# Kernel tuning notes

Measured on AMD Instinct MI355X. Metric: run time of the kernel, lower is better.

The kernel has to match this reference:

```python
import jax, jax.numpy as jnp
import numpy as np

CONF_THRES = 0.4
IOU_THRES = 0.45
MAX_WH = 4096.0   # class offset for class-aware NMS (agnostic=False)
MAX_DET = 300
B, N, NC = 8, 25200, 80


def setup_inputs() -> dict:
    key = jax.random.key(0)
    k1, k2, k3, k4, k5 = jax.random.split(key, 5)
    # realistic raw detector output: xywh in pixels, obj/cls scores in [0,1]
    xy = jax.random.uniform(k1, (B, N, 2), minval=0.0, maxval=608.0)
    wh = jax.random.uniform(k2, (B, N, 2), minval=4.0, maxval=96.0)
    obj = jax.random.uniform(k3, (B, N, 1))
    cls = jax.random.uniform(k4, (B, N, NC))
    prediction = jnp.concatenate([xy, wh, obj, cls], axis=-1)  # [B,N,85]
    logits = jax.random.normal(k5, (B, N, NC))
    return {"prediction": prediction, "logits": logits}


def _xywh2xyxy(b):
    cx, cy, w, h = b[..., 0], b[..., 1], b[..., 2], b[..., 3]
    return jnp.stack([cx - w / 2, cy - h / 2, cx + w / 2, cy + h / 2], axis=-1)


def _iou_one_vs_all(box, boxes):
    # box [4], boxes [N,4] -> IoU [N]
    lt = jnp.maximum(box[:2], boxes[:, :2])
    rb = jnp.minimum(box[2:], boxes[:, 2:])
    wh = jnp.clip(rb - lt, 0.0)
    inter = wh[:, 0] * wh[:, 1]
    a1 = (box[2] - box[0]) * (box[3] - box[1])
    a2 = (boxes[:, 2] - boxes[:, 0]) * (boxes[:, 3] - boxes[:, 1])
    return inter / (a1 + a2 - inter + 1e-9)


def _nms_image(pred, log_):
    # pred [N, 5+NC], log_ [N, NC]
    obj = pred[:, 4]
    scores_all = pred[:, 5:] * obj[:, None]          # x[:,5:] *= x[:,4:5]
    conf = scores_all.max(-1)                        # best-class conf
    cls = jnp.argmax(scores_all, -1)
    # obj-conf prefilter (xc mask) AND final conf filter, expressed as masking
    valid = (obj > CONF_THRES) & (conf > CONF_THRES)
    box = _xywh2xyxy(pred[:, :4])                    # [N,4]
    obox = box + (cls.astype(box.dtype) * MAX_WH)[:, None]  # class offset
    score0 = jnp.where(valid, conf, -1.0)

    def step(score_cur, _):
        idx = jnp.argmax(score_cur)
        keep = score_cur[idx] > 0.0
        iou = _iou_one_vs_all(obox[idx], obox)
        # suppress everything with IoU > thr (includes the picked box itself)
        new_score = jnp.where(keep & (iou > IOU_THRES), -1.0, score_cur)
        return new_score, (idx, keep)

    _, (idxs, keeps) = jax.lax.scan(step, score0, None, length=MAX_DET)
    m = keeps.astype(box.dtype)[:, None]
    dets = jnp.concatenate(
        [box[idxs], conf[idxs, None], cls[idxs, None].astype(box.dtype)], axis=-1
    ) * m                                            # [MAX_DET, 6], zero-padded
    return dets, log_[idxs] * m, keeps


def reference(prediction, logits):
    # returns (dets [B,300,6] = xyxy,conf,cls ; logits_sel [B,300,80] ; keep mask [B,300])
    return jax.vmap(_nms_image)(prediction, logits)
```

## Files before the change

kernel.cpp:

```cpp
#include <hip/hip_runtime.h>

#pragma clang fp contract(off)

#define NB 8
#define NN 25200
#define NCLS 80
#define NSTR 85
#define MAXDET 300
#define CONF_T 0.4f
#define IOU_T 0.45f
#define MAX_WH_C 4096.0f

#define NBIN 1024
#define BINSHIFT 14
#define BINBASE 0x3EC00000u
#define SELN 512
#define SORTN 2048

typedef unsigned long long ull;

__device__ __forceinline__ float cand_score(const float* __restrict__ p) {
    float obj = p[4];
    float best = p[5] * obj;
    for (int j = 1; j < NCLS; ++j) {
        float s = p[5 + j] * obj;
        if (s > best) best = s;
    }
    return ((obj > CONF_T) && (best > CONF_T)) ? best : -1.0f;
}
__device__ __forceinline__ int cand_cls(const float* __restrict__ p) {
    float obj = p[4];
    float best = p[5] * obj; int bc = 0;
    for (int j = 1; j < NCLS; ++j) {
        float s = p[5 + j] * obj;
        if (s > best) { best = s; bc = j; }
    }
    return bc;
}
__device__ __forceinline__ bool iou_gt(float ax1, float ay1, float ax2, float ay2, float aarea,
                                       float bx1, float by1, float bx2, float by2, float barea) {
    float lx = fmaxf(ax1, bx1);
    float ly = fmaxf(ay1, by1);
    float rx = fminf(ax2, bx2);
    float ry = fminf(ay2, by2);
    float iw = fmaxf(rx - lx, 0.0f);
    float ih = fmaxf(ry - ly, 0.0f);
    float inter = iw * ih;
    float iou = inter / ((aarea + barea - inter) + 1e-9f);
    return iou > IOU_T;
}

#define PREP_ROWS 64
__global__ __launch_bounds__(256) void prep_kernel(const float* __restrict__ pred,
                                                   float* __restrict__ score_ws) {
    __shared__ float st[PREP_ROWS * NSTR];
    const int R0 = blockIdx.x * PREP_ROWS;
    const float4* src = reinterpret_cast<const float4*>(pred + (size_t)R0 * NSTR);
    float4* dst4 = reinterpret_cast<float4*>(st);
    const int tid = threadIdx.x;
    for (int i = tid; i < PREP_ROWS * NSTR / 4; i += 256) dst4[i] = src[i];
    __syncthreads();

    int row = tid >> 2, part = tid & 3;
    const float* pr = st + row * NSTR;
    float obj = pr[4];
    float best = -1.0f;
    const float* pc = pr + 5 + part * 20;
#pragma unroll
    for (int k = 0; k < 20; ++k) {
        float s = pc[k] * obj;
        if (s > best) best = s;
    }
#pragma unroll
    for (int d = 1; d <= 2; d <<= 1) {
        float ob = __shfl_xor(best, d);
        if (ob > best) best = ob;
    }
    if (part == 0) {
        int grow = R0 + row;
        bool valid = (obj > CONF_T) && (best > CONF_T);
        score_ws[grow] = valid ? best : -1.0f;
    }
}

__global__ __launch_bounds__(1024) void selimg_kernel(const float* __restrict__ pred,
                                                      const float* __restrict__ score_ws,
                                                      int* __restrict__ cnt_ws, int* __restrict__ total_ws,
                                                      ull* __restrict__ sel_key,
                                                      float* __restrict__ sel_x1, float* __restrict__ sel_y1,
                                                      float* __restrict__ sel_x2, float* __restrict__ sel_y2,
                                                      float* __restrict__ sel_area, float* __restrict__ sel_cls,
                                                      int* __restrict__ sel_idx) {
    __shared__ int s_hist[NBIN];
    __shared__ ull s_key[SELN];
    __shared__ int s_gidx[SELN];
    __shared__ int s_cnt, s_T, s_total;

    const int b = blockIdx.x;
    const int tid = threadIdx.x;
    const int lane = tid & 63;
    const int wid = tid >> 6;
    const float* predb = pred + (size_t)b * NN * NSTR;
    const float* sb = score_ws + (size_t)b * NN;

    s_hist[tid] = 0;
    if (tid == 0) s_cnt = 0;
    __syncthreads();
    for (int g = tid; g < NN; g += 1024) {
        float s = sb[g];
        if (s > 0.0f) {
            int bin = (int)((__float_as_uint(s) - BINBASE) >> BINSHIFT);
            atomicAdd(&s_hist[bin], 1);
        }
    }
    __syncthreads();

    if (wid == 0) {
        int acc = 0; int S[16];
#pragma unroll
        for (int k = 15; k >= 0; --k) { acc += s_hist[lane * 16 + k]; S[k] = acc; }
        int tot = acc;
        int incl = tot;
#pragma unroll
        for (int d = 1; d < 64; d <<= 1) {
            int v = __shfl_down(incl, d);
            if (lane + d < 64) incl += v;
        }
        int E = incl - tot;
        int Tl = NBIN;
#pragma unroll
        for (int k = 0; k < 16; ++k)
            if (Tl == NBIN && S[k] + E <= SELN) Tl = lane * 16 + k;
        int total0 = incl;
#pragma unroll
        for (int d = 1; d < 64; d <<= 1) {
            int o = __shfl_xor(Tl, d);
            if (o < Tl) Tl = o;
        }
        if (lane == 0) { s_T = Tl; s_total = total0; }
    }
    __syncthreads();
    int T = s_T;

    for (int g = tid; g < NN; g += 1024) {
        float s = sb[g];
        if (s > 0.0f) {
            int bin = (int)((__float_as_uint(s) - BINBASE) >> BINSHIFT);
            if (bin >= T) {
                int pos = atomicAdd(&s_cnt, 1);
                if (pos < SELN) {
                    s_key[pos] = ((ull)__float_as_uint(s) << 32)
                                 | (unsigned int)(0xFFFFFFFFu - (unsigned int)g);
                    s_gidx[pos] = g;
                }
            }
        }
    }
    __syncthreads();
    int cnt = s_cnt; if (cnt > SELN) cnt = SELN;

    if (tid < cnt) {
        int g = s_gidx[tid];
        const float* p = predb + (size_t)g * NSTR;
        float cx = p[0], cy = p[1], w = p[2], h = p[3];
        int c = cand_cls(p);
        float off = (float)c * MAX_WH_C;
        float x1 = (cx - w * 0.5f) + off;
        float y1 = (cy - h * 0.5f) + off;
        float x2 = (cx + w * 0.5f) + off;
        float y2 = (cy + h * 0.5f) + off;
        int o = b * SELN + tid;
        sel_key[o] = s_key[tid];
        sel_x1[o] = x1; sel_y1[o] = y1; sel_x2[o] = x2; sel_y2[o] = y2;
        sel_area[o] = (x2 - x1) * (y2 - y1);
        sel_cls[o] = (float)c;
        sel_idx[o] = g;
    }
    if (tid == 0) { cnt_ws[b] = cnt; total_ws[b] = s_total; }
}

__global__ __launch_bounds__(256) void mask_kernel(const int* __restrict__ cnt_ws,
                                                   const ull* __restrict__ sel_key,
                                                   const float* __restrict__ sel_x1, const float* __restrict__ sel_y1,
                                                   const float* __restrict__ sel_x2, const float* __restrict__ sel_y2,
                                                   const float* __restrict__ sel_area,
                                                   ull* __restrict__ mask_ws) {
    __shared__ ull skey[SELN];
    __shared__ float ox1[SELN], oy1[SELN], ox2[SELN], oy2[SELN], oar[SELN];
    const int b = blockIdx.x >> 4;
    const int chunk = blockIdx.x & 15;
    const int tid = threadIdx.x;
    int cnt = cnt_ws[b]; if (cnt > SELN) cnt = SELN;
    for (int s = tid; s < SELN; s += 256) {
        if (s < cnt) {
            skey[s] = sel_key[b * SELN + s];
            ox1[s] = sel_x1[b * SELN + s]; oy1[s] = sel_y1[b * SELN + s];
            ox2[s] = sel_x2[b * SELN + s]; oy2[s] = sel_y2[b * SELN + s];
            oar[s] = sel_area[b * SELN + s];
        } else skey[s] = 0ull;
    }
    __syncthreads();
    int i = chunk * 32 + (tid & 31);
    int w = tid >> 5;
    if (i < cnt) {
        ull ki = skey[i];
        float ax1 = ox1[i], ay1 = oy1[i], ax2 = ox2[i], ay2 = oy2[i], aar = oar[i];
        ull m = 0ull;
        int jb = w << 6;
        int jend = cnt - jb; if (jend > 64) jend = 64;
        for (int t = 0; t < jend; ++t) {
            int j = jb + t;
            bool s = (skey[j] > ki) && iou_gt(ax1, ay1, ax2, ay2, aar,
                                             ox1[j], oy1[j], ox2[j], oy2[j], oar[j]);
            m |= (ull)s << t;
        }
        mask_ws[b * (8 * SELN) + w * SELN + i] = m;
    }
}

__global__ __launch_bounds__(1024) void resolve_kernel(
        const float* __restrict__ pred, const float* __restrict__ logits,
        const float* __restrict__ score_ws,
        const int* __restrict__ cnt_ws, const int* __restrict__ total_ws,
        const ull* __restrict__ mask_ws, const ull* __restrict__ sel_key,
        const float* __restrict__ sel_x1, const float* __restrict__ sel_y1,
        const float* __restrict__ sel_x2, const float* __restrict__ sel_y2,
        const float* __restrict__ sel_area, const float* __restrict__ sel_cls,
        const int* __restrict__ sel_idx,
        float* __restrict__ out) {
    __shared__ ull s_m[8][SELN];
    __shared__ ull s_key[SELN];
    __shared__ ull s_kw[8];
    __shared__ ull s_minkey;
    __shared__ float s_x1[SELN], s_y1[SELN], s_x2[SELN], s_y2[SELN], s_ar[SELN], s_cl[SELN];
    __shared__ int s_ix[SELN];
    __shared__ float kx1[MAXDET], ky1[MAXDET], kx2[MAXDET], ky2[MAXDET], kar[MAXDET];
    __shared__ float ksc[MAXDET], kcl[MAXDET];
    __shared__ int kix[MAXDET];
    __shared__ int s_kc;

    const int b = blockIdx.x;
    const int tid = threadIdx.x;
    const int lane = tid & 63;
    const int wid = tid >> 6;
    const float* predb = pred + (size_t)b * NN * NSTR;
    const float* logb  = logits + (size_t)b * NN * NCLS;
    const float* sb    = score_ws + (size_t)b * NN;

    int cnt = cnt_ws[b]; if (cnt > SELN) cnt = SELN;

    for (int i = tid; i < 8 * SELN; i += 1024)
        (&s_m[0][0])[i] = mask_ws[b * (8 * SELN) + i];
    for (int s = tid; s < SELN; s += 1024) {
        if (s < cnt) {
            s_key[s] = sel_key[b * SELN + s];
            s_x1[s] = sel_x1[b * SELN + s]; s_y1[s] = sel_y1[b * SELN + s];
            s_x2[s] = sel_x2[b * SELN + s]; s_y2[s] = sel_y2[b * SELN + s];
            s_ar[s] = sel_area[b * SELN + s]; s_cl[s] = sel_cls[b * SELN + s];
            s_ix[s] = sel_idx[b * SELN + s];
        } else s_key[s] = 0ull;
    }
    __syncthreads();

    if (wid == 0) {
        ull mk = ~0ull;
#pragma unroll
        for (int r = 0; r < 8; ++r) {
            int i = (r << 6) + lane;
            if (i < cnt) { ull k = s_key[i]; if (k < mk) mk = k; }
        }
#pragma unroll
        for (int d = 32; d >= 1; d >>= 1) {
            ull o = __shfl_xor(mk, d);
            if (o < mk) mk = o;
        }
        if (lane == 0) s_minkey = mk;

        ull vm[8], kw[8];
#pragma unroll
        for (int r = 0; r < 8; ++r) {
            int lo = r << 6;
            vm[r] = (cnt >= lo + 64) ? ~0ull : (cnt > lo ? ((1ull << (cnt - lo)) - 1ull) : 0ull);
            kw[r] = vm[r];
        }
        for (int round = 0; round < SELN; ++round) {
            ull nw[8];
#pragma unroll
            for (int r = 0; r < 8; ++r) {
                int i = (r << 6) + lane;
                ull supp = 0ull;
#pragma unroll
                for (int w = 0; w < 8; ++w) supp |= kw[w] & s_m[w][i];
                nw[r] = __ballot((int)(supp == 0ull)) & vm[r];
            }
            bool changed = false;
#pragma unroll
            for (int r = 0; r < 8; ++r) { changed |= (nw[r] != kw[r]); kw[r] = nw[r]; }
            if (!changed) break;
        }
        int totkept = 0;
#pragma unroll
        for (int r = 0; r < 8; ++r) totkept += __popcll(kw[r]);
        if (lane == 0) { s_kc = totkept < MAXDET ? totkept : MAXDET; }
        if (lane < 8) s_kw[lane] = kw[lane];
    }
    __syncthreads();
    int kc = s_kc;

    if (tid < SELN) {
        bool kept = (s_kw[tid >> 6] >> (tid & 63)) & 1ull;
        if (!kept) s_key[tid] = 0ull;
    }
    __syncthreads();

    {
        int i = tid >> 1, half = tid & 1;
        ull k = s_key[i];
        int r = 0;
        if (k != 0ull) {
            int jb = half << 8;
            for (int jj = 0; jj < 256; ++jj) {
                ull kj = s_key[jb + jj];
                r += (int)(kj > k);
            }
        }
        r += __shfl_xor(r, 1);
        if (half == 0 && k != 0ull && r < MAXDET) {
            kx1[r] = s_x1[i]; ky1[r] = s_y1[i]; kx2[r] = s_x2[i]; ky2[r] = s_y2[i];
            kar[r] = s_ar[i]; ksc[r] = __uint_as_float((unsigned int)(k >> 32));
            kcl[r] = s_cl[i]; kix[r] = s_ix[i];
        }
    }
    __syncthreads();

    if (wid == 0 && kc < MAXDET && total_ws[b] > cnt) {
        ull prevkey = (cnt > 0) ? s_minkey : ~0ull;
        while (kc < MAXDET) {
            ull best = 0ull;
            for (int i0 = lane; i0 < NN; i0 += 64) {
                float s = sb[i0];
                if (s > 0.0f) {
                    ull key = ((ull)__float_as_uint(s) << 32)
                              | (unsigned int)(0xFFFFFFFFu - (unsigned int)i0);
                    if (key < prevkey && key > best) best = key;
                }
            }
#pragma unroll
            for (int d = 32; d >= 1; d >>= 1) {
                ull o = __shfl_xor(best, d);
                if (o > best) best = o;
            }
            if (best == 0ull) break;
            prevkey = best;
            int gi = (int)(0xFFFFFFFFu - (unsigned int)(best & 0xFFFFFFFFull));
            float sc = __uint_as_float((unsigned int)(best >> 32));
            const float* pp = predb + (size_t)gi * NSTR;
            float cx = pp[0], cy = pp[1], w = pp[2], h = pp[3];
            int c = cand_cls(pp);
            float off = (float)c * MAX_WH_C;
            float x1 = (cx - w * 0.5f) + off;
            float y1 = (cy - h * 0.5f) + off;
            float x2 = (cx + w * 0.5f) + off;
            float y2 = (cy + h * 0.5f) + off;
            float ar = (x2 - x1) * (y2 - y1);
            bool f = false;
            for (int t = lane; t < kc; t += 64)
                if (iou_gt(kx1[t], ky1[t], kx2[t], ky2[t], kar[t], x1, y1, x2, y2, ar)) f = true;
            if (!__any((int)f)) {
                if (lane == 0) {
                    kx1[kc] = x1; ky1[kc] = y1; kx2[kc] = x2; ky2[kc] = y2;
                    kar[kc] = ar; ksc[kc] = sc; kcl[kc] = (float)c; kix[kc] = gi;
                }
                kc++;
            }
        }
        if (lane == 0) s_kc = kc;
    }
    __syncthreads();
    kc = s_kc;

    if (tid < MAXDET) {
        int t = tid;
        float o0 = 0, o1 = 0, o2 = 0, o3 = 0, o4 = 0, o5 = 0;
        if (t < kc) {
            int idx = kix[t];
            const float* pp = predb + (size_t)idx * NSTR;
            float cx = pp[0], cy = pp[1], w = pp[2], h = pp[3];
            o0 = cx - w * 0.5f; o1 = cy - h * 0.5f;
            o2 = cx + w * 0.5f; o3 = cy + h * 0.5f;
            o4 = ksc[t];        o5 = kcl[t];
        }
        float* dd = out + (size_t)b * (MAXDET * 6) + (size_t)t * 6;
        dd[0] = o0; dd[1] = o1; dd[2] = o2; dd[3] = o3; dd[4] = o4; dd[5] = o5;
        out[(size_t)NB * MAXDET * 6 + (size_t)NB * MAXDET * NCLS + (size_t)b * MAXDET + t] =
            (t < kc) ? 1.0f : 0.0f;
    }
    float* lbase = out + (size_t)NB * MAXDET * 6 + (size_t)b * (MAXDET * NCLS);
    for (int t = wid; t < MAXDET; t += 16) {
        float* dst = lbase + (size_t)t * NCLS;
        if (t < kc) {
            const float* src = logb + (size_t)kix[t] * NCLS;
            for (int c = lane; c < NCLS; c += 64) dst[c] = src[c];
        } else {
            for (int c = lane; c < NCLS; c += 64) dst[c] = 0.0f;
        }
    }
}

__global__ __launch_bounds__(1024) void fallback_kernel(const float* __restrict__ pred,
                                                        const float* __restrict__ logits,
                                                        float* __restrict__ out) {
    __shared__ ull s_keys[SORTN];
    __shared__ float sel_x1[SORTN], sel_y1[SORTN], sel_x2[SORTN], sel_y2[SORTN];
    __shared__ float sel_area[SORTN], sel_cls[SORTN];
    __shared__ int   sel_idx[SORTN];
    __shared__ float kx1[MAXDET], ky1[MAXDET], kx2[MAXDET], ky2[MAXDET], karea[MAXDET];
    __shared__ float kscore[MAXDET], kcls[MAXDET];
    __shared__ int   kidx[MAXDET];
    __shared__ int   s_hist[NBIN];
    __shared__ int   s_suppk[64];
    __shared__ unsigned int s_supmask[64][2];
    __shared__ int   s_kc, s_T, s_cnt;

    const int b = blockIdx.x;
    const int tid = threadIdx.x;
    const int lane = tid & 63;
    const int wid = tid >> 6;
    const float* predb = pred + (size_t)b * NN * NSTR;
    const float* logb  = logits + (size_t)b * NN * NCLS;

    int kc_total = 0;
    int prevT = NBIN;

    while (kc_total < MAXDET && prevT > 0) {
        s_hist[tid] = 0;
        if (tid == 0) { s_cnt = 0; s_T = NBIN; }
        __syncthreads();
        for (int i = tid; i < NN; i += 1024) {
            float s = cand_score(predb + (size_t)i * NSTR);
            if (s > 0.0f) {
                int bin = (int)((__float_as_uint(s) - BINBASE) >> BINSHIFT);
                if (bin < prevT) atomicAdd(&s_hist[bin], 1);
            }
        }
        __syncthreads();
        for (int d = 1; d < NBIN; d <<= 1) {
            int v = s_hist[tid] + ((tid + d < NBIN) ? s_hist[tid + d] : 0);
            __syncthreads();
            s_hist[tid] = v;
            __syncthreads();
        }
        if (s_hist[tid] <= SORTN) atomicMin(&s_T, tid);
        __syncthreads();
        int T = s_T;
        int rem_total = s_hist[0];
        if (T >= prevT) {
            if (rem_total == 0) { prevT = 0; break; }
            T = prevT - 1;
        }
        __syncthreads();
        for (int i = tid; i < NN; i += 1024) {
            float s = cand_score(predb + (size_t)i * NSTR);
            if (s > 0.0f) {
                int bin = (int)((__float_as_uint(s) - BINBASE) >> BINSHIFT);
                if (bin >= T && bin < prevT) {
                    int pos = atomicAdd(&s_cnt, 1);
                    if (pos < SORTN)
                        s_keys[pos] = ((ull)__float_as_uint(s) << 32)
                                      | (unsigned int)(0xFFFFFFFFu - (unsigned int)i);
                }
            }
        }
        __syncthreads();
        int cnt = s_cnt; if (cnt > SORTN) cnt = SORTN;
        int npow = 64; while (npow < cnt) npow <<= 1;
        for (int i = cnt + tid; i < npow; i += 1024) s_keys[i] = 0ull;
        __syncthreads();
        for (int k = 2; k <= npow; k <<= 1) {
            for (int j = k >> 1; j > 0; j >>= 1) {
                for (int idx = tid; idx < npow; idx += 1024) {
                    int p = idx ^ j;
                    if (p > idx) {
                        ull a = s_keys[idx], c = s_keys[p];
                        bool desc = ((idx & k) == 0);
                        if (desc ? (a < c) : (a > c)) { s_keys[idx] = c; s_keys[p] = a; }
                    }
                }
                __syncthreads();
            }
        }
        for (int t = tid; t < cnt; t += 1024) {
            ull key = s_keys[t];
            int i = (int)(0xFFFFFFFFu - (unsigned int)(key & 0xFFFFFFFFull));
            const float* p = predb + (size_t)i * NSTR;
            float cx = p[0], cy = p[1], w = p[2], h = p[3];
            int c = cand_cls(p);
            float off = (float)c * MAX_WH_C;
            float x1 = (cx - w * 0.5f) + off;
            float y1 = (cy - h * 0.5f) + off;
            float x2 = (cx + w * 0.5f) + off;
            float y2 = (cy + h * 0.5f) + off;
            sel_x1[t] = x1; sel_y1[t] = y1; sel_x2[t] = x2; sel_y2[t] = y2;
            sel_area[t] = (x2 - x1) * (y2 - y1);
            sel_cls[t] = (float)c;
            sel_idx[t] = i;
        }
        __syncthreads();
        int nb2 = (cnt + 63) >> 6;
        for (int batch = 0; batch < nb2; ++batch) {
            int kcb = kc_total;
            if (kcb >= MAXDET) break;
            if (tid < 64) { s_suppk[tid] = 0; s_supmask[tid][0] = 0u; s_supmask[tid][1] = 0u; }
            __syncthreads();

            int cloc = tid >> 4, ch = tid & 15;
            int gi = batch * 64 + cloc;
            bool validc = gi < cnt;
            float ax1 = 0, ay1 = 0, ax2 = 0, ay2 = 0, aar = 0;
            if (validc) {
                ax1 = sel_x1[gi]; ay1 = sel_y1[gi];
                ax2 = sel_x2[gi]; ay2 = sel_y2[gi]; aar = sel_area[gi];
            }
            bool flag = false;
            if (validc) {
                for (int t = ch; t < kcb; t += 16) {
                    if (iou_gt(kx1[t], ky1[t], kx2[t], ky2[t], karea[t],
                               ax1, ay1, ax2, ay2, aar)) flag = true;
                }
            }
            ull bal = __ballot((int)flag);
            if ((lane & 15) == 0) {
                unsigned int sub = (unsigned int)((bal >> (lane & 48)) & 0xFFFFull);
                s_suppk[cloc] = (sub != 0u);
            }
            unsigned int mbits = 0;
            if (validc) {
                for (int jj = 0; jj < 4; ++jj) {
                    int j = (ch << 2) + jj;
                    int gj = batch * 64 + j;
                    if (j > cloc && gj < cnt) {
                        if (iou_gt(ax1, ay1, ax2, ay2, aar,
                                   sel_x1[gj], sel_y1[gj], sel_x2[gj], sel_y2[gj], sel_area[gj]))
                            mbits |= 1u << (j & 31);
                    }
                }
            }
            if (mbits) atomicOr(&s_supmask[cloc][(ch >> 3) & 1], mbits);
            __syncthreads();

            if (wid == 0) {
                ull mask = ((ull)s_supmask[lane][1] << 32) | s_supmask[lane][0];
                bool validj = (batch * 64 + lane) < cnt;
                ull rem = __ballot((int)(validj && (s_suppk[lane] == 0)));
                ull keepbits = 0;
                int kcount = kcb;
                while (rem && kcount < MAXDET) {
                    int i = __builtin_ctzll(rem);
                    rem &= rem - 1;
                    keepbits |= 1ull << i;
                    ++kcount;
                    ull mi = __shfl(mask, i);
                    rem &= ~mi;
                }
                if ((keepbits >> lane) & 1ull) {
                    int pos = kcb + __popcll(keepbits & ((1ull << lane) - 1ull));
                    int g2 = batch * 64 + lane;
                    kx1[pos] = sel_x1[g2]; ky1[pos] = sel_y1[g2];
                    kx2[pos] = sel_x2[g2]; ky2[pos] = sel_y2[g2];
                    karea[pos] = sel_area[g2];
                    kcls[pos] = sel_cls[g2]; kidx[pos] = sel_idx[g2];
                    kscore[pos] = __uint_as_float((unsigned int)(s_keys[g2] >> 32));
                }
                if (lane == 0) s_kc = kcount;
            }
            __syncthreads();
            kc_total = s_kc;
            __syncthreads();
        }
        prevT = T;
    }

    __syncthreads();
    int kc = kc_total;
    if (tid < MAXDET) {
        int t = tid;
        float o0 = 0, o1 = 0, o2 = 0, o3 = 0, o4 = 0, o5 = 0;
        if (t < kc) {
            int idx = kidx[t];
            const float* pp = predb + (size_t)idx * NSTR;
            float cx = pp[0], cy = pp[1], w = pp[2], h = pp[3];
            o0 = cx - w * 0.5f; o1 = cy - h * 0.5f;
            o2 = cx + w * 0.5f; o3 = cy + h * 0.5f;
            o4 = kscore[t];     o5 = kcls[t];
        }
        float* dd = out + (size_t)b * (MAXDET * 6) + (size_t)t * 6;
        dd[0] = o0; dd[1] = o1; dd[2] = o2; dd[3] = o3; dd[4] = o4; dd[5] = o5;
        out[(size_t)NB * MAXDET * 6 + (size_t)NB * MAXDET * NCLS + (size_t)b * MAXDET + t] =
            (t < kc) ? 1.0f : 0.0f;
    }
    float* lbase = out + (size_t)NB * MAXDET * 6 + (size_t)b * (MAXDET * NCLS);
    for (int t = wid; t < MAXDET; t += 16) {
        float* dst = lbase + (size_t)t * NCLS;
        if (t < kc) {
            const float* src = logb + (size_t)kidx[t] * NCLS;
            for (int c = lane; c < NCLS; c += 64) dst[c] = src[c];
        } else {
            for (int c = lane; c < NCLS; c += 64) dst[c] = 0.0f;
        }
    }
}

extern "C" void kernel_launch(void* const* d_in, const int* in_sizes, int n_in,
                              void* d_out, int out_size, void* d_ws, size_t ws_size,
                              hipStream_t stream) {
    const float* pred   = (const float*)d_in[0];
    const float* logits = (const float*)d_in[1];
    float* out = (float*)d_out;

    const size_t off_mask = 0;
    const size_t off_key  = 262144;
    const size_t off_flt  = 294912;
    const size_t off_idx  = off_flt + 6 * 16384;
    const size_t off_cnt  = off_idx + 16384;
    const size_t off_tot  = off_cnt + 64;
    const size_t off_sws  = off_tot + 64;
    const size_t need     = off_sws + (size_t)NB * NN * 4;

    if (d_ws == nullptr || ws_size < need) {
        fallback_kernel<<<NB, 1024, 0, stream>>>(pred, logits, out);
        return;
    }

    char* ws = (char*)d_ws;
    ull* mask_ws = (ull*)(ws + off_mask);
    ull* sel_key = (ull*)(ws + off_key);
    float* sel_x1 = (float*)(ws + off_flt);
    float* sel_y1 = sel_x1 + NB * SELN;
    float* sel_x2 = sel_y1 + NB * SELN;
    float* sel_y2 = sel_x2 + NB * SELN;
    float* sel_area = sel_y2 + NB * SELN;
    float* sel_cls = sel_area + NB * SELN;
    int*   sel_idx = (int*)(ws + off_idx);
    int*   cnt_ws = (int*)(ws + off_cnt);
    int*   total_ws = (int*)(ws + off_tot);
    float* score_ws = (float*)(ws + off_sws);

    prep_kernel<<<(NB * NN) / PREP_ROWS, 256, 0, stream>>>(pred, score_ws);
    selimg_kernel<<<NB, 1024, 0, stream>>>(pred, score_ws, cnt_ws, total_ws, sel_key,
                                           sel_x1, sel_y1, sel_x2, sel_y2,
                                           sel_area, sel_cls, sel_idx);
    mask_kernel<<<NB * 16, 256, 0, stream>>>(cnt_ws, sel_key,
                                             sel_x1, sel_y1, sel_x2, sel_y2, sel_area, mask_ws);
    resolve_kernel<<<NB, 1024, 0, stream>>>(pred, logits, score_ws, cnt_ws, total_ws,
                                            mask_ws, sel_key,
                                            sel_x1, sel_y1, sel_x2, sel_y2,
                                            sel_area, sel_cls, sel_idx, out);
}
```

Before: 87.82 us.

## Fuse NMS pipeline into single cooperative persistent kernel with grid syncs

```diff
diff --git a/kernel.cpp b/kernel.cpp
--- a/kernel.cpp
+++ b/kernel.cpp
@@ -1,4 +1,5 @@
 #include <hip/hip_runtime.h>
+#include <hip/hip_cooperative_groups.h>
 
 #pragma clang fp contract(off)
 
@@ -16,8 +17,12 @@
 #define BINBASE 0x3EC00000u
 #define SELN 512
 #define SORTN 2048
+#define PREP_ROWS 64
+#define COOP_GRID 256
+#define COOP_BLK 256
 
 typedef unsigned long long ull;
+namespace cg = cooperative_groups;
 
 __device__ __forceinline__ float cand_score(const float* __restrict__ p) {
     float obj = p[4];
@@ -50,7 +55,351 @@
     return iou > IOU_T;
 }
 
-#define PREP_ROWS 64
+struct Params {
+    const float* pred; const float* logits;
+    float* score; int* hist; int* cnt; int* total;
+    ull* key; float* x1; float* y1; float* x2; float* y2; float* ar; float* cl; int* ix;
+    ull* mask; int* kix; float* ksc; float* kcl; int* kcnt;
+    float* out;
+};
+
+struct SMemA { float stage[PREP_ROWS * NSTR]; };
+struct SMemD { ull key[SELN]; float x1[SELN], y1[SELN], x2[SELN], y2[SELN], ar[SELN]; };
+struct SMemE {
+    ull m[8][SELN]; ull key[SELN];
+    float x1[SELN], y1[SELN], x2[SELN], y2[SELN], ar[SELN], cl[SELN];
+    int ix[SELN];
+    float kx1[MAXDET], ky1[MAXDET], kx2[MAXDET], ky2[MAXDET], kar[MAXDET], ksc[MAXDET], kcl[MAXDET];
+    int kix[MAXDET];
+};
+union SMem { SMemA a; SMemD d; SMemE e; };
+
+__global__ __launch_bounds__(COOP_BLK) void coop_kernel(Params P) {
+    __shared__ SMem sm;
+    __shared__ int sT, sTot, s_kc;
+    __shared__ ull s_kw[8];
+    __shared__ ull s_minkey;
+
+    cg::grid_group grid = cg::this_grid();
+    const int tid = threadIdx.x;
+    const int bx = blockIdx.x;
+
+    {
+        int gt = bx * COOP_BLK + tid;
+        for (int i = gt; i < NB * NBIN + NB; i += COOP_GRID * COOP_BLK) {
+            if (i < NB * NBIN) P.hist[i] = 0;
+            else P.cnt[i - NB * NBIN] = 0;
+        }
+    }
+    grid.sync();
+
+    for (int tile = bx; tile < (NB * NN) / PREP_ROWS; tile += COOP_GRID) {
+        const float4* src = reinterpret_cast<const float4*>(P.pred + (size_t)tile * PREP_ROWS * NSTR);
+        float4* dst4 = reinterpret_cast<float4*>(sm.a.stage);
+        for (int i = tid; i < PREP_ROWS * NSTR / 4; i += COOP_BLK) dst4[i] = src[i];
+        __syncthreads();
+        int row = tid >> 2, part = tid & 3;
+        const float* pr = sm.a.stage + row * NSTR;
+        float obj = pr[4];
+        float best = -1.0f;
+        const float* pc = pr + 5 + part * 20;
+#pragma unroll
+        for (int k = 0; k < 20; ++k) {
+            float s = pc[k] * obj;
+            if (s > best) best = s;
+        }
+#pragma unroll
+        for (int d = 1; d <= 2; d <<= 1) {
+            float ob = __shfl_xor(best, d);
+            if (ob > best) best = ob;
+        }
+        if (part == 0) {
+            int grow = tile * PREP_ROWS + row;
+            bool valid = (obj > CONF_T) && (best > CONF_T);
+            P.score[grow] = valid ? best : -1.0f;
+            if (valid) {
+                int ib = grow / NN;
+                int bin = (int)((__float_as_uint(best) - BINBASE) >> BINSHIFT);
+                atomicAdd(&P.hist[ib * NBIN + bin], 1);
+            }
+        }
+        __syncthreads();
+    }
+    grid.sync();
+
+    {
+        const int img = bx >> 5;
+        const int sub = bx & 31;
+        if (tid < 64) {
+            int lane = tid;
+            int acc = 0; int S[16];
+#pragma unroll
+            for (int k = 15; k >= 0; --k) { acc += P.hist[img * NBIN + lane * 16 + k]; S[k] = acc; }
+            int tot = acc;
+            int incl = tot;
+#pragma unroll
+            for (int d = 1; d < 64; d <<= 1) {
+                int v = __shfl_down(incl, d);
+                if (lane + d < 64) incl += v;
+            }
+            int E = incl - tot;
+            int Tl = NBIN;
+#pragma unroll
+            for (int k = 0; k < 16; ++k)
+                if (Tl == NBIN && S[k] + E <= SELN) Tl = lane * 16 + k;
+            int total0 = incl;
+#pragma unroll
+            for (int d = 1; d < 64; d <<= 1) {
+                int o = __shfl_xor(Tl, d);
+                if (o < Tl) Tl = o;
+            }
+            if (lane == 0) { sT = Tl; sTot = total0; }
+        }
+        __syncthreads();
+        int T = sT;
+        if (sub == 0 && tid == 0) P.total[img] = sTot;
+        const float* sb = P.score + (size_t)img * NN;
+        const float* predb = P.pred + (size_t)img * NN * NSTR;
+        int g0 = sub * 788;
+        int g1 = g0 + 788; if (g1 > NN) g1 = NN;
+        for (int g = g0 + tid; g < g1; g += COOP_BLK) {
+            float s = sb[g];
+            if (s > 0.0f) {
+                int bin = (int)((__float_as_uint(s) - BINBASE) >> BINSHIFT);
+                if (bin >= T) {
+                    int pos = atomicAdd(&P.cnt[img], 1);
+                    if (pos < SELN) {
+                        int o = img * SELN + pos;
+                        const float* p = predb + (size_t)g * NSTR;
+                        float cx = p[0], cy = p[1], w = p[2], h = p[3];
+                        int c = cand_cls(p);
+                        float off = (float)c * MAX_WH_C;
+                        float x1 = (cx - w * 0.5f) + off;
+                        float y1 = (cy - h * 0.5f) + off;
+                        float x2 = (cx + w * 0.5f) + off;
+                        float y2 = (cy + h * 0.5f) + off;
+                        P.key[o] = ((ull)__float_as_uint(s) << 32)
+                                   | (unsigned int)(0xFFFFFFFFu - (unsigned int)g);
+                        P.x1[o] = x1; P.y1[o] = y1; P.x2[o] = x2; P.y2[o] = y2;
+                        P.ar[o] = (x2 - x1) * (y2 - y1);
+                        P.cl[o] = (float)c; P.ix[o] = g;
+                    }
+                }
+            }
+        }
+    }
+    grid.sync();
+
+    if (bx < NB * 16) {
+        const int b = bx >> 4;
+        const int chunk = bx & 15;
+        int cntb = P.cnt[b]; if (cntb > SELN) cntb = SELN;
+        for (int s = tid; s < SELN; s += COOP_BLK) {
+            if (s < cntb) {
+                sm.d.key[s] = P.key[b * SELN + s];
+                sm.d.x1[s] = P.x1[b * SELN + s]; sm.d.y1[s] = P.y1[b * SELN + s];
+                sm.d.x2[s] = P.x2[b * SELN + s]; sm.d.y2[s] = P.y2[b * SELN + s];
+                sm.d.ar[s] = P.ar[b * SELN + s];
+            } else sm.d.key[s] = 0ull;
+        }
+        __syncthreads();
+        int i = chunk * 32 + (tid & 31);
+        int w = tid >> 5;
+        if (i < cntb) {
+            ull ki = sm.d.key[i];
+            float ax1 = sm.d.x1[i], ay1 = sm.d.y1[i], ax2 = sm.d.x2[i], ay2 = sm.d.y2[i], aar = sm.d.ar[i];
+            ull m = 0ull;
+            int jb = w << 6;
+            int jend = cntb - jb; if (jend > 64) jend = 64;
+            for (int t = 0; t < jend; ++t) {
+                int j = jb + t;
+                bool s = (sm.d.key[j] > ki) && iou_gt(ax1, ay1, ax2, ay2, aar,
+                                                     sm.d.x1[j], sm.d.y1[j], sm.d.x2[j], sm.d.y2[j], sm.d.ar[j]);
+                m |= (ull)s << t;
+            }
+            P.mask[b * (8 * SELN) + w * SELN + i] = m;
+        }
+    }
+    grid.sync();
+
+    if (bx < NB) {
+        const int b = bx;
+        const int lane = tid & 63;
+        const int wid = tid >> 6;
+        const float* predb = P.pred + (size_t)b * NN * NSTR;
+        const float* sb = P.score + (size_t)b * NN;
+        int cnt = P.cnt[b]; if (cnt > SELN) cnt = SELN;
+
+        for (int i = tid; i < 8 * SELN; i += COOP_BLK)
+            (&sm.e.m[0][0])[i] = P.mask[b * (8 * SELN) + i];
+        for (int s = tid; s < SELN; s += COOP_BLK) {
+            if (s < cnt) {
+                sm.e.key[s] = P.key[b * SELN + s];
+                sm.e.x1[s] = P.x1[b * SELN + s]; sm.e.y1[s] = P.y1[b * SELN + s];
+                sm.e.x2[s] = P.x2[b * SELN + s]; sm.e.y2[s] = P.y2[b * SELN + s];
+                sm.e.ar[s] = P.ar[b * SELN + s]; sm.e.cl[s] = P.cl[b * SELN + s];
+                sm.e.ix[s] = P.ix[b * SELN + s];
+            } else sm.e.key[s] = 0ull;
+        }
+        __syncthreads();
+
+        if (wid == 0) {
+            ull mk = ~0ull;
+#pragma unroll
+            for (int r = 0; r < 8; ++r) {
+                int i = (r << 6) + lane;
+                if (i < cnt) { ull k = sm.e.key[i]; if (k < mk) mk = k; }
+            }
+#pragma unroll
+            for (int d = 32; d >= 1; d >>= 1) {
+                ull o = __shfl_xor(mk, d);
+                if (o < mk) mk = o;
+            }
+            if (lane == 0) s_minkey = mk;
+
+            ull vm[8], kw[8];
+#pragma unroll
+            for (int r = 0; r < 8; ++r) {
+                int lo = r << 6;
+                vm[r] = (cnt >= lo + 64) ? ~0ull : (cnt > lo ? ((1ull << (cnt - lo)) - 1ull) : 0ull);
+                kw[r] = vm[r];
+            }
+            for (int round = 0; round < SELN; ++round) {
+                ull nw[8];
+#pragma unroll
+                for (int r = 0; r < 8; ++r) {
+                    int i = (r << 6) + lane;
+                    ull supp = 0ull;
+#pragma unroll
+                    for (int w = 0; w < 8; ++w) supp |= kw[w] & sm.e.m[w][i];
+                    nw[r] = __ballot((int)(supp == 0ull)) & vm[r];
+                }
+                bool changed = false;
+#pragma unroll
+                for (int r = 0; r < 8; ++r) { changed |= (nw[r] != kw[r]); kw[r] = nw[r]; }
+                if (!changed) break;
+            }
+            int totkept = 0;
+#pragma unroll
+            for (int r = 0; r < 8; ++r) totkept += __popcll(kw[r]);
+            if (lane == 0) s_kc = totkept < MAXDET ? totkept : MAXDET;
+            if (lane < 8) s_kw[lane] = kw[lane];
+        }
+        __syncthreads();
+        int kc = s_kc;
+
+        for (int s = tid; s < SELN; s += COOP_BLK) {
+            bool kept = (s_kw[s >> 6] >> (s & 63)) & 1ull;
+            if (!kept) sm.e.key[s] = 0ull;
+        }
+        __syncthreads();
+
+        for (int ii = tid; ii < SELN; ii += COOP_BLK) {
+            ull k = sm.e.key[ii];
+            if (k != 0ull) {
+                int r = 0;
+                for (int j = 0; j < SELN; ++j) r += (int)(sm.e.key[j] > k);
+                if (r < MAXDET) {
+                    sm.e.kx1[r] = sm.e.x1[ii]; sm.e.ky1[r] = sm.e.y1[ii];
+                    sm.e.kx2[r] = sm.e.x2[ii]; sm.e.ky2[r] = sm.e.y2[ii];
+                    sm.e.kar[r] = sm.e.ar[ii];
+                    sm.e.ksc[r] = __uint_as_float((unsigned int)(k >> 32));
+                    sm.e.kcl[r] = sm.e.cl[ii]; sm.e.kix[r] = sm.e.ix[ii];
+                }
+            }
+        }
+        __syncthreads();
+
+        if (wid == 0 && kc < MAXDET && P.total[b] > cnt) {
+            ull prevkey = (cnt > 0) ? s_minkey : ~0ull;
+            while (kc < MAXDET) {
+                ull best = 0ull;
+                for (int i0 = lane; i0 < NN; i0 += 64) {
+                    float s = sb[i0];
+                    if (s > 0.0f) {
+                        ull key = ((ull)__float_as_uint(s) << 32)
+                                  | (unsigned int)(0xFFFFFFFFu - (unsigned int)i0);
+                        if (key < prevkey && key > best) best = key;
+                    }
+                }
+#pragma unroll
+                for (int d = 32; d >= 1; d >>= 1) {
+                    ull o = __shfl_xor(best, d);
+                    if (o > best) best = o;
+                }
+                if (best == 0ull) break;
+                prevkey = best;
+                int gi = (int)(0xFFFFFFFFu - (unsigned int)(best & 0xFFFFFFFFull));
+                float sc = __uint_as_float((unsigned int)(best >> 32));
+                const float* pp = predb + (size_t)gi * NSTR;
+                float cx = pp[0], cy = pp[1], w = pp[2], h = pp[3];
+                int c = cand_cls(pp);
+                float off = (float)c * MAX_WH_C;
+                float x1 = (cx - w * 0.5f) + off;
+                float y1 = (cy - h * 0.5f) + off;
+                float x2 = (cx + w * 0.5f) + off;
+                float y2 = (cy + h * 0.5f) + off;
+                float ar = (x2 - x1) * (y2 - y1);
+                bool f = false;
+                for (int t = lane; t < kc; t += 64)
+                    if (iou_gt(sm.e.kx1[t], sm.e.ky1[t], sm.e.kx2[t], sm.e.ky2[t], sm.e.kar[t],
+                               x1, y1, x2, y2, ar)) f = true;
+                if (!__any((int)f)) {
+                    if (lane == 0) {
+                        sm.e.kx1[kc] = x1; sm.e.ky1[kc] = y1; sm.e.kx2[kc] = x2; sm.e.ky2[kc] = y2;
+                        sm.e.kar[kc] = ar; sm.e.ksc[kc] = sc; sm.e.kcl[kc] = (float)c; sm.e.kix[kc] = gi;
+                    }
+                    kc++;
+                }
+            }
+            if (lane == 0) s_kc = kc;
+        }
+        __syncthreads();
+        kc = s_kc;
+
+        for (int t = tid; t < kc; t += COOP_BLK) {
+            P.kix[b * MAXDET + t] = sm.e.kix[t];
+            P.ksc[b * MAXDET + t] = sm.e.ksc[t];
+            P.kcl[b * MAXDET + t] = sm.e.kcl[t];
+        }
+        if (tid == 0) P.kcnt[b] = kc;
+    }
+    grid.sync();
+
+    {
+        int gt = bx * COOP_BLK + tid;
+        for (int item = gt; item < NB * MAXDET; item += COOP_GRID * COOP_BLK) {
+            int b = item / MAXDET, t = item - b * MAXDET;
+            int kc = P.kcnt[b];
+            float o0 = 0, o1 = 0, o2 = 0, o3 = 0, o4 = 0, o5 = 0, keep = 0;
+            if (t < kc) {
+                int idx = P.kix[b * MAXDET + t];
+                const float* pp = P.pred + ((size_t)b * NN + idx) * NSTR;
+                float cx = pp[0], cy = pp[1], w = pp[2], h = pp[3];
+                o0 = cx - w * 0.5f; o1 = cy - h * 0.5f;
+                o2 = cx + w * 0.5f; o3 = cy + h * 0.5f;
+                o4 = P.ksc[b * MAXDET + t]; o5 = P.kcl[b * MAXDET + t];
+                keep = 1.0f;
+            }
+            float* dd = P.out + (size_t)b * (MAXDET * 6) + (size_t)t * 6;
+            dd[0] = o0; dd[1] = o1; dd[2] = o2; dd[3] = o3; dd[4] = o4; dd[5] = o5;
+            P.out[(size_t)NB * MAXDET * 6 + (size_t)NB * MAXDET * NCLS + (size_t)b * MAXDET + t] = keep;
+        }
+        for (int item = gt; item < NB * MAXDET * NCLS; item += COOP_GRID * COOP_BLK) {
+            int b = item / (MAXDET * NCLS);
+            int rem = item - b * (MAXDET * NCLS);
+            int t = rem / NCLS;
+            int kc = P.kcnt[b];
+            float v = 0.0f;
+            if (t < kc) {
+                int c = rem - t * NCLS;
+                v = P.logits[((size_t)b * NN + P.kix[b * MAXDET + t]) * NCLS + c];
+            }
+            P.out[(size_t)NB * MAXDET * 6 + (size_t)b * (MAXDET * NCLS) + rem] = v;
+        }
+    }
+}
+
 __global__ __launch_bounds__(256) void prep_kernel(const float* __restrict__ pred,
                                                    float* __restrict__ score_ws) {
     __shared__ float st[PREP_ROWS * NSTR];
@@ -60,7 +409,6 @@
     const int tid = threadIdx.x;
     for (int i = tid; i < PREP_ROWS * NSTR / 4; i += 256) dst4[i] = src[i];
     __syncthreads();
-
     int row = tid >> 2, part = tid & 3;
     const float* pr = st + row * NSTR;
     float obj = pr[4];
@@ -95,7 +443,6 @@
     __shared__ ull s_key[SELN];
     __shared__ int s_gidx[SELN];
     __shared__ int s_cnt, s_T, s_total;
-
     const int b = blockIdx.x;
     const int tid = threadIdx.x;
     const int lane = tid & 63;
@@ -114,7 +461,6 @@
         }
     }
     __syncthreads();
-
     if (wid == 0) {
         int acc = 0; int S[16];
 #pragma unroll
@@ -141,7 +487,6 @@
     }
     __syncthreads();
     int T = s_T;
-
     for (int g = tid; g < NN; g += 1024) {
         float s = sb[g];
         if (s > 0.0f) {
@@ -158,7 +503,6 @@
     }
     __syncthreads();
     int cnt = s_cnt; if (cnt > SELN) cnt = SELN;
-
     if (tid < cnt) {
         int g = s_gidx[tid];
         const float* p = predb + (size_t)g * NSTR;
@@ -301,7 +645,7 @@
         int totkept = 0;
 #pragma unroll
         for (int r = 0; r < 8; ++r) totkept += __popcll(kw[r]);
-        if (lane == 0) { s_kc = totkept < MAXDET ? totkept : MAXDET; }
+        if (lane == 0) s_kc = totkept < MAXDET ? totkept : MAXDET;
         if (lane < 8) s_kw[lane] = kw[lane];
     }
     __syncthreads();
@@ -512,7 +856,6 @@
             if (kcb >= MAXDET) break;
             if (tid < 64) { s_suppk[tid] = 0; s_supmask[tid][0] = 0u; s_supmask[tid][1] = 0u; }
             __syncthreads();
-
             int cloc = tid >> 4, ch = tid & 15;
             int gi = batch * 64 + cloc;
             bool validc = gi < cnt;
@@ -547,7 +890,6 @@
             }
             if (mbits) atomicOr(&s_supmask[cloc][(ch >> 3) & 1], mbits);
             __syncthreads();
-
             if (wid == 0) {
                 ull mask = ((ull)s_supmask[lane][1] << 32) | s_supmask[lane][0];
                 bool validj = (batch * 64 + lane) < cnt;
@@ -617,14 +959,19 @@
     const float* logits = (const float*)d_in[1];
     float* out = (float*)d_out;
 
-    const size_t off_mask = 0;
-    const size_t off_key  = 262144;
-    const size_t off_flt  = 294912;
-    const size_t off_idx  = off_flt + 6 * 16384;
-    const size_t off_cnt  = off_idx + 16384;
-    const size_t off_tot  = off_cnt + 64;
-    const size_t off_sws  = off_tot + 64;
-    const size_t need     = off_sws + (size_t)NB * NN * 4;
+    const size_t off_mask  = 0;
+    const size_t off_key   = 262144;
+    const size_t off_score = 294912;
+    const size_t off_flt   = 1101312;
+    const size_t off_ix    = off_flt + 6 * 16384;
+    const size_t off_hist  = off_ix + 16384;
+    const size_t off_cnt   = off_hist + 32768;
+    const size_t off_tot   = off_cnt + 32;
+    const size_t off_kix   = off_tot + 32;
+    const size_t off_ksc   = off_kix + 9600;
+    const size_t off_kcl   = off_ksc + 9600;
+    const size_t off_kcnt  = off_kcl + 9600;
+    const size_t need      = off_kcnt + 32;
 
     if (d_ws == nullptr || ws_size < need) {
         fallback_kernel<<<NB, 1024, 0, stream>>>(pred, logits, out);
@@ -632,18 +979,43 @@
     }
 
     char* ws = (char*)d_ws;
-    ull* mask_ws = (ull*)(ws + off_mask);
-    ull* sel_key = (ull*)(ws + off_key);
+    ull*   mask_ws = (ull*)(ws + off_mask);
+    ull*   sel_key = (ull*)(ws + off_key);
+    float* score_ws = (float*)(ws + off_score);
     float* sel_x1 = (float*)(ws + off_flt);
     float* sel_y1 = sel_x1 + NB * SELN;
     float* sel_x2 = sel_y1 + NB * SELN;
     float* sel_y2 = sel_x2 + NB * SELN;
     float* sel_area = sel_y2 + NB * SELN;
     float* sel_cls = sel_area + NB * SELN;
-    int*   sel_idx = (int*)(ws + off_idx);
+    int*   sel_idx = (int*)(ws + off_ix);
+    int*   hist = (int*)(ws + off_hist);
     int*   cnt_ws = (int*)(ws + off_cnt);
     int*   total_ws = (int*)(ws + off_tot);
-    float* score_ws = (float*)(ws + off_sws);
+    int*   kix_ws = (int*)(ws + off_kix);
+    float* ksc_ws = (float*)(ws + off_ksc);
+    float* kcl_ws = (float*)(ws + off_kcl);
+    int*   kcnt_ws = (int*)(ws + off_kcnt);
+
+    int dev = 0;
+    hipGetDevice(&dev);
+    int coop = 0;
+    hipDeviceGetAttribute(&coop, hipDeviceAttributeCooperativeLaunch, dev);
+
+    if (coop) {
+        Params p;
+        p.pred = pred; p.logits = logits;
+        p.score = score_ws; p.hist = hist; p.cnt = cnt_ws; p.total = total_ws;
+        p.key = sel_key; p.x1 = sel_x1; p.y1 = sel_y1; p.x2 = sel_x2; p.y2 = sel_y2;
+        p.ar = sel_area; p.cl = sel_cls; p.ix = sel_idx;
+        p.mask = mask_ws; p.kix = kix_ws; p.ksc = ksc_ws; p.kcl = kcl_ws; p.kcnt = kcnt_ws;
+        p.out = out;
+        void* args[] = { &p };
+        hipError_t e = hipLaunchCooperativeKernel((const void*)coop_kernel,
+                                                  dim3(COOP_GRID), dim3(COOP_BLK),
+                                                  args, 0, stream);
+        if (e == hipSuccess) return;
+    }
 
     prep_kernel<<<(NB * NN) / PREP_ROWS, 256, 0, stream>>>(pred, score_ws);
     selimg_kernel<<<NB, 1024, 0, stream>>>(pred, score_ws, cnt_ws, total_ws, sel_key,
```

After: 250.2 us. 2.85x slower.

## Fuse candidate selection into mask kernel with redundant per-chunk selection

Applied to the files above, without the earlier changes.

```diff
diff --git a/kernel.cpp b/kernel.cpp
--- a/kernel.cpp
+++ b/kernel.cpp
@@ -16,6 +16,7 @@
 #define BINBASE 0x3EC00000u
 #define SELN 512
 #define SORTN 2048
+#define PREP_ROWS 64
 
 typedef unsigned long long ull;
 
@@ -50,7 +51,6 @@
     return iou > IOU_T;
 }
 
-#define PREP_ROWS 64
 __global__ __launch_bounds__(256) void prep_kernel(const float* __restrict__ pred,
                                                    float* __restrict__ score_ws) {
     __shared__ float st[PREP_ROWS * NSTR];
@@ -83,30 +83,32 @@
     }
 }
 
-__global__ __launch_bounds__(1024) void selimg_kernel(const float* __restrict__ pred,
-                                                      const float* __restrict__ score_ws,
-                                                      int* __restrict__ cnt_ws, int* __restrict__ total_ws,
-                                                      ull* __restrict__ sel_key,
-                                                      float* __restrict__ sel_x1, float* __restrict__ sel_y1,
-                                                      float* __restrict__ sel_x2, float* __restrict__ sel_y2,
-                                                      float* __restrict__ sel_area, float* __restrict__ sel_cls,
-                                                      int* __restrict__ sel_idx) {
+#define SELRNG 99
+__global__ __launch_bounds__(256) void selmask_kernel(const float* __restrict__ pred,
+        const float* __restrict__ score_ws,
+        int* __restrict__ cnt_ws, int* __restrict__ total_ws,
+        ull* __restrict__ sel_key,
+        float* __restrict__ sel_x1, float* __restrict__ sel_y1,
+        float* __restrict__ sel_x2, float* __restrict__ sel_y2,
+        float* __restrict__ sel_area, float* __restrict__ sel_cls,
+        int* __restrict__ sel_idx,
+        ull* __restrict__ mask_ws) {
     __shared__ int s_hist[NBIN];
+    __shared__ int s_c[256], s_off[256];
     __shared__ ull s_key[SELN];
     __shared__ int s_gidx[SELN];
-    __shared__ int s_cnt, s_T, s_total;
-
-    const int b = blockIdx.x;
+    __shared__ float m_x1[SELN], m_y1[SELN], m_x2[SELN], m_y2[SELN], m_ar[SELN], m_cl[SELN];
+    __shared__ int sT, sTot, sSel;
+
+    const int b = blockIdx.x >> 4;
+    const int chunk = blockIdx.x & 15;
     const int tid = threadIdx.x;
-    const int lane = tid & 63;
-    const int wid = tid >> 6;
+    const float* sb = score_ws + (size_t)b * NN;
     const float* predb = pred + (size_t)b * NN * NSTR;
-    const float* sb = score_ws + (size_t)b * NN;
-
-    s_hist[tid] = 0;
-    if (tid == 0) s_cnt = 0;
-    __syncthreads();
-    for (int g = tid; g < NN; g += 1024) {
+
+    for (int i = tid; i < NBIN; i += 256) s_hist[i] = 0;
+    __syncthreads();
+    for (int g = tid; g < NN; g += 256) {
         float s = sb[g];
         if (s > 0.0f) {
             int bin = (int)((__float_as_uint(s) - BINBASE) >> BINSHIFT);
@@ -115,7 +117,8 @@
     }
     __syncthreads();
 
-    if (wid == 0) {
+    if (tid < 64) {
+        int lane = tid;
         int acc = 0; int S[16];
 #pragma unroll
         for (int k = 15; k >= 0; --k) { acc += s_hist[lane * 16 + k]; S[k] = acc; }
@@ -137,84 +140,101 @@
             int o = __shfl_xor(Tl, d);
             if (o < Tl) Tl = o;
         }
-        if (lane == 0) { s_T = Tl; s_total = total0; }
-    }
-    __syncthreads();
-    int T = s_T;
-
-    for (int g = tid; g < NN; g += 1024) {
+        if (lane == 0) { sT = Tl; sTot = total0; }
+    }
+    __syncthreads();
+    int T = sT;
+
+    int g0 = tid * SELRNG;
+    int g1 = g0 + SELRNG; if (g1 > NN) g1 = NN;
+    int c = 0;
+    for (int g = g0; g < g1; ++g) {
         float s = sb[g];
-        if (s > 0.0f) {
-            int bin = (int)((__float_as_uint(s) - BINBASE) >> BINSHIFT);
-            if (bin >= T) {
-                int pos = atomicAdd(&s_cnt, 1);
-                if (pos < SELN) {
-                    s_key[pos] = ((ull)__float_as_uint(s) << 32)
-                                 | (unsigned int)(0xFFFFFFFFu - (unsigned int)g);
-                    s_gidx[pos] = g;
-                }
-            }
-        }
-    }
-    __syncthreads();
-    int cnt = s_cnt; if (cnt > SELN) cnt = SELN;
-
-    if (tid < cnt) {
-        int g = s_gidx[tid];
+        if (s > 0.0f && (int)((__float_as_uint(s) - BINBASE) >> BINSHIFT) >= T) ++c;
+    }
+    s_c[tid] = c;
+    __syncthreads();
+    if (tid < 64) {
+        int base = tid << 2;
+        int a0 = s_c[base], a1 = s_c[base + 1], a2 = s_c[base + 2], a3 = s_c[base + 3];
+        int l0 = a0, l1 = l0 + a1, l2 = l1 + a2, l3 = l2 + a3;
+        int inc = l3;
+        int lane = tid;
+#pragma unroll
+        for (int d = 1; d < 64; d <<= 1) {
+            int v = __shfl_up(inc, d);
+            if (lane >= d) inc += v;
+        }
+        int ex = inc - l3;
+        s_off[base] = ex;
+        s_off[base + 1] = ex + l0;
+        s_off[base + 2] = ex + l1;
+        s_off[base + 3] = ex + l2;
+        if (lane == 63) sSel = ex + l3;
+    }
+    __syncthreads();
+    {
+        int r = s_off[tid];
+        for (int g = g0; g < g1; ++g) {
+            float s = sb[g];
+            if (s > 0.0f && (int)((__float_as_uint(s) - BINBASE) >> BINSHIFT) >= T) {
+                if (r < SELN) {
+                    s_key[r] = ((ull)__float_as_uint(s) << 32)
+                               | (unsigned int)(0xFFFFFFFFu - (unsigned int)g);
+                    s_gidx[r] = g;
+                }
+                ++r;
+            }
+        }
+    }
+    __syncthreads();
+    int cnt = sSel; if (cnt > SELN) cnt = SELN;
+
+    for (int s = tid; s < cnt; s += 256) {
+        int g = s_gidx[s];
         const float* p = predb + (size_t)g * NSTR;
         float cx = p[0], cy = p[1], w = p[2], h = p[3];
-        int c = cand_cls(p);
-        float off = (float)c * MAX_WH_C;
+        int cc = cand_cls(p);
+        float off = (float)cc * MAX_WH_C;
         float x1 = (cx - w * 0.5f) + off;
         float y1 = (cy - h * 0.5f) + off;
         float x2 = (cx + w * 0.5f) + off;
         float y2 = (cy + h * 0.5f) + off;
-        int o = b * SELN + tid;
-        sel_key[o] = s_key[tid];
-        sel_x1[o] = x1; sel_y1[o] = y1; sel_x2[o] = x2; sel_y2[o] = y2;
-        sel_area[o] = (x2 - x1) * (y2 - y1);
-        sel_cls[o] = (float)c;
-        sel_idx[o] = g;
-    }
-    if (tid == 0) { cnt_ws[b] = cnt; total_ws[b] = s_total; }
-}
-
-__global__ __launch_bounds__(256) void mask_kernel(const int* __restrict__ cnt_ws,
-                                                   const ull* __restrict__ sel_key,
-                                                   const float* __restrict__ sel_x1, const float* __restrict__ sel_y1,
-                                                   const float* __restrict__ sel_x2, const float* __restrict__ sel_y2,
-                                                   const float* __restrict__ sel_area,
-                                                   ull* __restrict__ mask_ws) {
-    __shared__ ull skey[SELN];
-    __shared__ float ox1[SELN], oy1[SELN], ox2[SELN], oy2[SELN], oar[SELN];
-    const int b = blockIdx.x >> 4;
-    const int chunk = blockIdx.x & 15;
-    const int tid = threadIdx.x;
-    int cnt = cnt_ws[b]; if (cnt > SELN) cnt = SELN;
-    for (int s = tid; s < SELN; s += 256) {
-        if (s < cnt) {
-            skey[s] = sel_key[b * SELN + s];
-            ox1[s] = sel_x1[b * SELN + s]; oy1[s] = sel_y1[b * SELN + s];
-            ox2[s] = sel_x2[b * SELN + s]; oy2[s] = sel_y2[b * SELN + s];
-            oar[s] = sel_area[b * SELN + s];
-        } else skey[s] = 0ull;
-    }
-    __syncthreads();
-    int i = chunk * 32 + (tid & 31);
-    int w = tid >> 5;
-    if (i < cnt) {
-        ull ki = skey[i];
-        float ax1 = ox1[i], ay1 = oy1[i], ax2 = ox2[i], ay2 = oy2[i], aar = oar[i];
-        ull m = 0ull;
-        int jb = w << 6;
-        int jend = cnt - jb; if (jend > 64) jend = 64;
-        for (int t = 0; t < jend; ++t) {
-            int j = jb + t;
-            bool s = (skey[j] > ki) && iou_gt(ax1, ay1, ax2, ay2, aar,
-                                             ox1[j], oy1[j], ox2[j], oy2[j], oar[j]);
-            m |= (ull)s << t;
-        }
-        mask_ws[b * (8 * SELN) + w * SELN + i] = m;
+        m_x1[s] = x1; m_y1[s] = y1; m_x2[s] = x2; m_y2[s] = y2;
+        m_ar[s] = (x2 - x1) * (y2 - y1);
+        m_cl[s] = (float)cc;
+    }
+    __syncthreads();
+
+    {
+        int i = chunk * 32 + (tid & 31);
+        int w = tid >> 5;
+        if (i < cnt) {
+            ull ki = s_key[i];
+            float ax1 = m_x1[i], ay1 = m_y1[i], ax2 = m_x2[i], ay2 = m_y2[i], aar = m_ar[i];
+            ull m = 0ull;
+            int jb = w << 6;
+            int jend = cnt - jb; if (jend > 64) jend = 64;
+            for (int t = 0; t < jend; ++t) {
+                int j = jb + t;
+                bool sres = (s_key[j] > ki) && iou_gt(ax1, ay1, ax2, ay2, aar,
+                                                     m_x1[j], m_y1[j], m_x2[j], m_y2[j], m_ar[j]);
+                m |= (ull)sres << t;
+            }
+            mask_ws[b * (8 * SELN) + w * SELN + i] = m;
+        }
+    }
+
+    if (chunk == 0) {
+        for (int s = tid; s < cnt; s += 256) {
+            int o = b * SELN + s;
+            sel_key[o] = s_key[s];
+            sel_x1[o] = m_x1[s]; sel_y1[o] = m_y1[s];
+            sel_x2[o] = m_x2[s]; sel_y2[o] = m_y2[s];
+            sel_area[o] = m_ar[s]; sel_cls[o] = m_cl[s];
+            sel_idx[o] = s_gidx[s];
+        }
+        if (tid == 0) { cnt_ws[b] = cnt; total_ws[b] = sTot; }
     }
 }
 
@@ -301,7 +321,7 @@
         int totkept = 0;
 #pragma unroll
         for (int r = 0; r < 8; ++r) totkept += __popcll(kw[r]);
-        if (lane == 0) { s_kc = totkept < MAXDET ? totkept : MAXDET; }
+        if (lane == 0) s_kc = totkept < MAXDET ? totkept : MAXDET;
         if (lane < 8) s_kw[lane] = kw[lane];
     }
     __syncthreads();
@@ -512,7 +532,6 @@
             if (kcb >= MAXDET) break;
             if (tid < 64) { s_suppk[tid] = 0; s_supmask[tid][0] = 0u; s_supmask[tid][1] = 0u; }
             __syncthreads();
-
             int cloc = tid >> 4, ch = tid & 15;
             int gi = batch * 64 + cloc;
             bool validc = gi < cnt;
@@ -547,7 +566,6 @@
             }
             if (mbits) atomicOr(&s_supmask[cloc][(ch >> 3) & 1], mbits);
             __syncthreads();
-
             if (wid == 0) {
                 ull mask = ((ull)s_supmask[lane][1] << 32) | s_supmask[lane][0];
                 bool validj = (batch * 64 + lane) < cnt;
@@ -617,14 +635,14 @@
     const float* logits = (const float*)d_in[1];
     float* out = (float*)d_out;
 
-    const size_t off_mask = 0;
-    const size_t off_key  = 262144;
-    const size_t off_flt  = 294912;
-    const size_t off_idx  = off_flt + 6 * 16384;
-    const size_t off_cnt  = off_idx + 16384;
-    const size_t off_tot  = off_cnt + 64;
-    const size_t off_sws  = off_tot + 64;
-    const size_t need     = off_sws + (size_t)NB * NN * 4;
+    const size_t off_mask  = 0;
+    const size_t off_key   = 262144;
+    const size_t off_score = 294912;
+    const size_t off_flt   = 1101312;
+    const size_t off_ix    = off_flt + 6 * 16384;
+    const size_t off_cnt   = off_ix + 16384;
+    const size_t off_tot   = off_cnt + 32;
+    const size_t need      = off_tot + 32;
 
     if (d_ws == nullptr || ws_size < need) {
         fallback_kernel<<<NB, 1024, 0, stream>>>(pred, logits, out);
@@ -632,25 +650,23 @@
     }
 
     char* ws = (char*)d_ws;
-    ull* mask_ws = (ull*)(ws + off_mask);
-    ull* sel_key = (ull*)(ws + off_key);
+    ull*   mask_ws = (ull*)(ws + off_mask);
+    ull*   sel_key = (ull*)(ws + off_key);
+    float* score_ws = (float*)(ws + off_score);
     float* sel_x1 = (float*)(ws + off_flt);
     float* sel_y1 = sel_x1 + NB * SELN;
     float* sel_x2 = sel_y1 + NB * SELN;
     float* sel_y2 = sel_x2 + NB * SELN;
     float* sel_area = sel_y2 + NB * SELN;
     float* sel_cls = sel_area + NB * SELN;
-    int*   sel_idx = (int*)(ws + off_idx);
+    int*   sel_idx = (int*)(ws + off_ix);
     int*   cnt_ws = (int*)(ws + off_cnt);
     int*   total_ws = (int*)(ws + off_tot);
-    float* score_ws = (float*)(ws + off_sws);
 
     prep_kernel<<<(NB * NN) / PREP_ROWS, 256, 0, stream>>>(pred, score_ws);
-    selimg_kernel<<<NB, 1024, 0, stream>>>(pred, score_ws, cnt_ws, total_ws, sel_key,
-                                           sel_x1, sel_y1, sel_x2, sel_y2,
-                                           sel_area, sel_cls, sel_idx);
-    mask_kernel<<<NB * 16, 256, 0, stream>>>(cnt_ws, sel_key,
-                                             sel_x1, sel_y1, sel_x2, sel_y2, sel_area, mask_ws);
+    selmask_kernel<<<NB * 16, 256, 0, stream>>>(pred, score_ws, cnt_ws, total_ws, sel_key,
+                                                sel_x1, sel_y1, sel_x2, sel_y2,
+                                                sel_area, sel_cls, sel_idx, mask_ws);
     resolve_kernel<<<NB, 1024, 0, stream>>>(pred, logits, score_ws, cnt_ws, total_ws,
                                             mask_ws, sel_key,
                                             sel_x1, sel_y1, sel_x2, sel_y2,
```

Measured after the change: 131.1 us. +49.3%, slower.
